# Optimization experiments

Hardware: AMD Instinct MI355X
Metric: run time of the kernel (lower is better)

The kernel has to match this reference:

```python
import jax, jax.numpy as jnp
import numpy as np

NUM_BLOCKS = 4
BLOCK_SIZE = 2048
BATCH = 512
NUM_ITERATIONS = 2
# static tridiagonal block sparsity pattern: (out_block_i, in_block_j)
BLOCK_PAIRS = [(0, 0), (0, 1), (1, 0), (1, 1), (1, 2), (2, 1), (2, 2), (2, 3), (3, 2), (3, 3)]


def setup_inputs() -> dict:
    key = jax.random.key(0)
    kx, kw, kb = jax.random.split(key, 3)
    X = jax.random.normal(kx, (NUM_BLOCKS, BATCH, BLOCK_SIZE), dtype=jnp.float32)
    # torch nn.Linear default init: U(-1/sqrt(fan_in), 1/sqrt(fan_in))
    bound = 1.0 / np.sqrt(BLOCK_SIZE)
    W = jax.random.uniform(kw, (len(BLOCK_PAIRS), BLOCK_SIZE, BLOCK_SIZE),
                           minval=-bound, maxval=bound, dtype=jnp.float32)
    b = jax.random.uniform(kb, (len(BLOCK_PAIRS), BLOCK_SIZE),
                           minval=-bound, maxval=bound, dtype=jnp.float32)
    return {"X": X, "W": W, "b": b}


def reference(X, W, b):
    # X: [num_blocks, batch, block_size]
    # W: [n_present_blocks, out_feat, in_feat], b: [n_present_blocks, out_feat]
    # Each iteration: y_i = relu( sum_{j : (i,j) present} x_j @ W_ij^T + b_ij )
    for _ in range(NUM_ITERATIONS):
        Y = jnp.zeros_like(X)
        for k, (i, j) in enumerate(BLOCK_PAIRS):  # small static set of block GEMMs
            Y = Y.at[i].add(jnp.einsum('be,oe->bo', X[j], W[k]) + b[k])
        X = jax.nn.relu(Y)
    return X
```

## Files before the change

kernel.cpp:

```cpp
#include <hip/hip_runtime.h>
#include <cstdint>
#include <cstddef>

typedef __bf16 bf16;
typedef bf16 bf16x4 __attribute__((ext_vector_type(4)));
typedef bf16 bf16x8 __attribute__((ext_vector_type(8)));
typedef float f32x4 __attribute__((ext_vector_type(4)));

#define NB 4
#define BATCH 512
#define BS 2048
#define NPAIRS 10

__constant__ int c_npairs[NB]   = {2, 3, 3, 2};
__constant__ int c_pj[NB][3]    = {{0, 1, 0}, {0, 1, 2}, {1, 2, 3}, {2, 3, 0}};
__constant__ int c_pk[NB][3]    = {{0, 1, 0}, {2, 3, 4}, {5, 6, 7}, {8, 9, 0}};

__global__ __launch_bounds__(256) void convert_kernel(
    const float* __restrict__ X, const float* __restrict__ W,
    const float* __restrict__ b,
    bf16* __restrict__ Xbf, bf16* __restrict__ Wbf, float* __restrict__ bias4)
{
    const int nW4 = NPAIRS * BS * BS / 4;
    const int nX4 = NB * BATCH * BS / 4;
    int idx    = blockIdx.x * blockDim.x + threadIdx.x;
    int stride = gridDim.x * blockDim.x;
    const float4* W4 = (const float4*)W;
    const float4* X4 = (const float4*)X;
    for (int i = idx; i < nW4; i += stride) {
        float4 v = W4[i];
        bf16x4 o = { (bf16)v.x, (bf16)v.y, (bf16)v.z, (bf16)v.w };
        *(bf16x4*)(Wbf + 4 * (size_t)i) = o;
    }
    for (int i = idx; i < nX4; i += stride) {
        float4 v = X4[i];
        bf16x4 o = { (bf16)v.x, (bf16)v.y, (bf16)v.z, (bf16)v.w };
        *(bf16x4*)(Xbf + 4 * (size_t)i) = o;
    }
    if (idx < NB * BS) {
        int i = idx >> 11;
        int o = idx & (BS - 1);
        float s = 0.f;
        int np = c_npairs[i];
        for (int p = 0; p < np; ++p) s += b[c_pk[i][p] * BS + o];
        bias4[idx] = s;
    }
}

typedef __attribute__((address_space(1))) void void_g;
typedef __attribute__((address_space(3))) void void_l;

__device__ __forceinline__ void gload16(const bf16* g, bf16* l)
{
    __builtin_amdgcn_global_load_lds((void_g*)g, (void_l*)l, 16, 0, 0);
}

__global__ __launch_bounds__(256, 2) void block_gemm(
    const bf16* __restrict__ Xbf,
    const bf16* __restrict__ Wbf,
    const float* __restrict__ bias4,
    bf16* __restrict__ Xnext,
    float* __restrict__ Yout,
    int write_f32)
{
    __shared__ bf16 sA[128 * 32];
    __shared__ bf16 sB[128 * 32];

    const int tid  = threadIdx.x;
    const int lane = tid & 63;
    const int wid  = tid >> 6;
    const int wm   = (wid & 1) * 64;
    const int wn   = (wid >> 1) * 64;
    const int ib   = blockIdx.z;
    const int bm0  = blockIdx.y * 128;
    const int bn0  = blockIdx.x * 128;

    f32x4 acc[4][4];
    const f32x4 zero = {0.f, 0.f, 0.f, 0.f};
#pragma unroll
    for (int i = 0; i < 4; ++i)
#pragma unroll
        for (int j = 0; j < 4; ++j) acc[i][j] = zero;

    const int srow = tid >> 2;
    const int skp  = (tid & 3) * 8;
    bf16* ldsA0 = sA + (size_t)tid * 8;
    bf16* ldsA1 = sA + 2048 + (size_t)tid * 8;
    bf16* ldsB0 = sB + (size_t)tid * 8;
    bf16* ldsB1 = sB + 2048 + (size_t)tid * 8;

    const int lm = lane & 15;
    const int lk = (lane >> 4) * 8;

    const int np = c_npairs[ib];
    for (int p = 0; p < np; ++p) {
        const bf16* Ab = Xbf + ((size_t)c_pj[ib][p] * BATCH + bm0 + srow) * BS + skp;
        const bf16* Bb = Wbf + ((size_t)c_pk[ib][p] * BS    + bn0 + srow) * BS + skp;
        for (int k0 = 0; k0 < BS; k0 += 32) {
            __syncthreads();
            gload16(Ab + k0,            ldsA0);
            gload16(Ab + 64 * BS + k0,  ldsA1);
            gload16(Bb + k0,            ldsB0);
            gload16(Bb + 64 * BS + k0,  ldsB1);
            __syncthreads();

            bf16x8 af[4], bfr[4];
#pragma unroll
            for (int mi = 0; mi < 4; ++mi)
                af[mi] = *(const bf16x8*)(sA + (wm + mi * 16 + lm) * 32 + lk);
#pragma unroll
            for (int ni = 0; ni < 4; ++ni)
                bfr[ni] = *(const bf16x8*)(sB + (wn + ni * 16 + lm) * 32 + lk);
#pragma unroll
            for (int mi = 0; mi < 4; ++mi)
#pragma unroll
                for (int ni = 0; ni < 4; ++ni)
                    acc[mi][ni] = __builtin_amdgcn_mfma_f32_16x16x32_bf16(
                        af[mi], bfr[ni], acc[mi][ni], 0, 0, 0);
        }
    }

    const float* bias = bias4 + ib * BS;
#pragma unroll
    for (int mi = 0; mi < 4; ++mi) {
#pragma unroll
        for (int ni = 0; ni < 4; ++ni) {
            const int m = bm0 + wm + mi * 16 + (lane >> 4) * 4;
            const int n = bn0 + wn + ni * 16 + lm;
            const float bv = bias[n];
            const size_t base = ((size_t)ib * BATCH + m) * BS + n;
            if (write_f32) {
#pragma unroll
                for (int r = 0; r < 4; ++r) {
                    float v = acc[mi][ni][r] + bv;
                    Yout[base + (size_t)r * BS] = v > 0.f ? v : 0.f;
                }
            } else {
#pragma unroll
                for (int r = 0; r < 4; ++r) {
                    float v = acc[mi][ni][r] + bv;
                    v = v > 0.f ? v : 0.f;
                    Xnext[base + (size_t)r * BS] = (bf16)v;
                }
            }
        }
    }
}

extern "C" void kernel_launch(void* const* d_in, const int* in_sizes, int n_in,
                              void* d_out, int out_size, void* d_ws, size_t ws_size,
                              hipStream_t stream)
{
    const float* X = (const float*)d_in[0];
    const float* W = (const float*)d_in[1];
    const float* b = (const float*)d_in[2];
    float* out = (float*)d_out;
    char* ws = (char*)d_ws;

    const size_t W_BYTES = (size_t)NPAIRS * BS * BS * 2;
    const size_t X_BYTES = (size_t)NB * BATCH * BS * 2;

    bf16*  Wbf   = (bf16*)ws;
    bf16*  Xbf0  = (bf16*)(ws + W_BYTES);
    bf16*  Xbf1  = (bf16*)(ws + W_BYTES + X_BYTES);
    float* bias4 = (float*)(ws + W_BYTES + 2 * X_BYTES);

    hipLaunchKernelGGL(convert_kernel, dim3(4096), dim3(256), 0, stream,
                       X, W, b, Xbf0, Wbf, bias4);

    dim3 grid(BS / 128, BATCH / 128, NB);
    hipLaunchKernelGGL(block_gemm, grid, dim3(256), 0, stream,
                       Xbf0, Wbf, bias4, Xbf1, (float*)nullptr, 0);
    hipLaunchKernelGGL(block_gemm, grid, dim3(256), 0, stream,
                       Xbf1, Wbf, bias4, (bf16*)nullptr, out, 1);
}
```

Baseline: 470.5 us.

## Split-K GEMM with in-kernel fp32 W conversion and double-buffered LDS

Drops the separate fp32-to-bf16 conversion pass over W. The GEMM now reads fp32 W directly and converts it in registers before storing to LDS. The K dimension is split four ways, giving four times as many workgroups to fill the device, and the LDS staging is double-buffered so the next tile's loads overlap the current MFMAs. A new combine kernel sums the partials and applies bias and ReLU. The cost is a large fp32 partial buffer written and re-read every iteration, and W is read twice in fp32 instead of once in fp32 plus twice in bf16.

```diff
diff --git a/kernel.cpp b/kernel.cpp
--- a/kernel.cpp
+++ b/kernel.cpp
@@ -10,39 +10,27 @@
 #define NB 4
 #define BATCH 512
 #define BS 2048
-#define NPAIRS 10
-
-__constant__ int c_npairs[NB]   = {2, 3, 3, 2};
-__constant__ int c_pj[NB][3]    = {{0, 1, 0}, {0, 1, 2}, {1, 2, 3}, {2, 3, 0}};
-__constant__ int c_pk[NB][3]    = {{0, 1, 0}, {2, 3, 4}, {5, 6, 7}, {8, 9, 0}};
-
-__global__ __launch_bounds__(256) void convert_kernel(
-    const float* __restrict__ X, const float* __restrict__ W,
-    const float* __restrict__ b,
-    bf16* __restrict__ Xbf, bf16* __restrict__ Wbf, float* __restrict__ bias4)
-{
-    const int nW4 = NPAIRS * BS * BS / 4;
-    const int nX4 = NB * BATCH * BS / 4;
-    int idx    = blockIdx.x * blockDim.x + threadIdx.x;
-    int stride = gridDim.x * blockDim.x;
-    const float4* W4 = (const float4*)W;
-    const float4* X4 = (const float4*)X;
-    for (int i = idx; i < nW4; i += stride) {
-        float4 v = W4[i];
-        bf16x4 o = { (bf16)v.x, (bf16)v.y, (bf16)v.z, (bf16)v.w };
-        *(bf16x4*)(Wbf + 4 * (size_t)i) = o;
-    }
-    for (int i = idx; i < nX4; i += stride) {
-        float4 v = X4[i];
-        bf16x4 o = { (bf16)v.x, (bf16)v.y, (bf16)v.z, (bf16)v.w };
-        *(bf16x4*)(Xbf + 4 * (size_t)i) = o;
-    }
+#define KQ 4
+#define KSPAN (BS / KQ)
+
+__constant__ int c_npairs[NB] = {2, 3, 3, 2};
+__constant__ int c_pj[NB][3]  = {{0, 1, 0}, {0, 1, 2}, {1, 2, 3}, {2, 3, 0}};
+__constant__ int c_pk[NB][3]  = {{0, 1, 0}, {2, 3, 4}, {5, 6, 7}, {8, 9, 0}};
+
+__global__ __launch_bounds__(256) void xcvt_kernel(
+    const float* __restrict__ X, const float* __restrict__ b,
+    bf16* __restrict__ Xbf, float* __restrict__ bias4)
+{
+    const int idx = blockIdx.x * 256 + threadIdx.x;
+    float4 v = ((const float4*)X)[idx];
+    bf16x4 o = { (bf16)v.x, (bf16)v.y, (bf16)v.z, (bf16)v.w };
+    *(bf16x4*)(Xbf + 4 * (size_t)idx) = o;
     if (idx < NB * BS) {
         int i = idx >> 11;
-        int o = idx & (BS - 1);
+        int o2 = idx & (BS - 1);
         float s = 0.f;
         int np = c_npairs[i];
-        for (int p = 0; p < np; ++p) s += b[c_pk[i][p] * BS + o];
+        for (int p = 0; p < np; ++p) s += b[c_pk[i][p] * BS + o2];
         bias4[idx] = s;
     }
 }
@@ -50,30 +38,41 @@
 typedef __attribute__((address_space(1))) void void_g;
 typedef __attribute__((address_space(3))) void void_l;
 
-__device__ __forceinline__ void gload16(const bf16* g, bf16* l)
-{
-    __builtin_amdgcn_global_load_lds((void_g*)g, (void_l*)l, 16, 0, 0);
-}
-
-__global__ __launch_bounds__(256, 2) void block_gemm(
+__global__ __launch_bounds__(256, 4) void gemm_ksplit(
     const bf16* __restrict__ Xbf,
-    const bf16* __restrict__ Wbf,
-    const float* __restrict__ bias4,
-    bf16* __restrict__ Xnext,
-    float* __restrict__ Yout,
-    int write_f32)
-{
-    __shared__ bf16 sA[128 * 32];
-    __shared__ bf16 sB[128 * 32];
+    const float* __restrict__ W,
+    float* __restrict__ P)
+{
+    __shared__ bf16 sA[2][128 * 32];
+    __shared__ bf16 sB[2][128 * 32];
 
     const int tid  = threadIdx.x;
     const int lane = tid & 63;
     const int wid  = tid >> 6;
     const int wm   = (wid & 1) * 64;
     const int wn   = (wid >> 1) * 64;
-    const int ib   = blockIdx.z;
+    const int z    = blockIdx.z;
+    const int ib   = z >> 2;
+    const int kq   = z & 3;
     const int bm0  = blockIdx.y * 128;
     const int bn0  = blockIdx.x * 128;
+    const int np     = c_npairs[ib];
+    const int nsteps = np * (KSPAN / 32);
+
+    const int a_row = tid >> 2;
+    const int a_kp  = (tid & 3) * 8;
+    const int b_row = tid >> 1;
+    const int b_kp  = (tid & 1) * 16;
+
+    const bf16* A_0 = Xbf + ((size_t)c_pj[ib][0] * BATCH + bm0 + a_row) * BS + kq * KSPAN + a_kp;
+    const bf16* A_1 = Xbf + ((size_t)c_pj[ib][1] * BATCH + bm0 + a_row) * BS + kq * KSPAN + a_kp;
+    const bf16* A_2 = Xbf + ((size_t)c_pj[ib][2] * BATCH + bm0 + a_row) * BS + kq * KSPAN + a_kp;
+    const float* B_0 = W + ((size_t)c_pk[ib][0] * BS + bn0 + b_row) * BS + kq * KSPAN + b_kp;
+    const float* B_1 = W + ((size_t)c_pk[ib][1] * BS + bn0 + b_row) * BS + kq * KSPAN + b_kp;
+    const float* B_2 = W + ((size_t)c_pk[ib][2] * BS + bn0 + b_row) * BS + kq * KSPAN + b_kp;
+
+    const int lm = lane & 15;
+    const int lk = (lane >> 4) * 8;
 
     f32x4 acc[4][4];
     const f32x4 zero = {0.f, 0.f, 0.f, 0.f};
@@ -82,68 +81,104 @@
 #pragma unroll
         for (int j = 0; j < 4; ++j) acc[i][j] = zero;
 
-    const int srow = tid >> 2;
-    const int skp  = (tid & 3) * 8;
-    bf16* ldsA0 = sA + (size_t)tid * 8;
-    bf16* ldsA1 = sA + 2048 + (size_t)tid * 8;
-    bf16* ldsB0 = sB + (size_t)tid * 8;
-    bf16* ldsB1 = sB + 2048 + (size_t)tid * 8;
-
-    const int lm = lane & 15;
-    const int lk = (lane >> 4) * 8;
-
-    const int np = c_npairs[ib];
-    for (int p = 0; p < np; ++p) {
-        const bf16* Ab = Xbf + ((size_t)c_pj[ib][p] * BATCH + bm0 + srow) * BS + skp;
-        const bf16* Bb = Wbf + ((size_t)c_pk[ib][p] * BS    + bn0 + srow) * BS + skp;
-        for (int k0 = 0; k0 < BS; k0 += 32) {
-            __syncthreads();
-            gload16(Ab + k0,            ldsA0);
-            gload16(Ab + 64 * BS + k0,  ldsA1);
-            gload16(Bb + k0,            ldsB0);
-            gload16(Bb + 64 * BS + k0,  ldsB1);
-            __syncthreads();
-
-            bf16x8 af[4], bfr[4];
-#pragma unroll
-            for (int mi = 0; mi < 4; ++mi)
-                af[mi] = *(const bf16x8*)(sA + (wm + mi * 16 + lm) * 32 + lk);
+    float4 br0, br1, br2, br3;
+
+    auto stageA = [&](int s, int buf) {
+        const int p = s >> 4;
+        const bf16* Ab = (p == 0) ? A_0 : ((p == 1) ? A_1 : A_2);
+        Ab += (s & 15) * 32;
+        bf16* l = &sA[buf][tid * 8];
+        __builtin_amdgcn_global_load_lds((void_g*)Ab, (void_l*)l, 16, 0, 0);
+        __builtin_amdgcn_global_load_lds((void_g*)(Ab + 64 * BS), (void_l*)(l + 2048), 16, 0, 0);
+    };
+    auto loadB = [&](int s) {
+        const int p = s >> 4;
+        const float* Bb = (p == 0) ? B_0 : ((p == 1) ? B_1 : B_2);
+        Bb += (s & 15) * 32;
+        br0 = *(const float4*)(Bb);
+        br1 = *(const float4*)(Bb + 4);
+        br2 = *(const float4*)(Bb + 8);
+        br3 = *(const float4*)(Bb + 12);
+    };
+    auto commitB = [&](int buf) {
+        bf16x8 w0 = { (bf16)br0.x, (bf16)br0.y, (bf16)br0.z, (bf16)br0.w,
+                      (bf16)br1.x, (bf16)br1.y, (bf16)br1.z, (bf16)br1.w };
+        bf16x8 w1 = { (bf16)br2.x, (bf16)br2.y, (bf16)br2.z, (bf16)br2.w,
+                      (bf16)br3.x, (bf16)br3.y, (bf16)br3.z, (bf16)br3.w };
+        *(bf16x8*)(&sB[buf][b_row * 32 + b_kp])     = w0;
+        *(bf16x8*)(&sB[buf][b_row * 32 + b_kp + 8]) = w1;
+    };
+
+    stageA(0, 0);
+    loadB(0);
+    commitB(0);
+
+    int cur = 0;
+    for (int s = 0; s < nsteps; ++s) {
+        __syncthreads();
+        if (s + 1 < nsteps) {
+            stageA(s + 1, cur ^ 1);
+            loadB(s + 1);
+        }
+        bf16x8 af[4], bfr[4];
+#pragma unroll
+        for (int mi = 0; mi < 4; ++mi)
+            af[mi] = *(const bf16x8*)(&sA[cur][(wm + mi * 16 + lm) * 32 + lk]);
+#pragma unroll
+        for (int ni = 0; ni < 4; ++ni)
+            bfr[ni] = *(const bf16x8*)(&sB[cur][(wn + ni * 16 + lm) * 32 + lk]);
+#pragma unroll
+        for (int mi = 0; mi < 4; ++mi)
 #pragma unroll
             for (int ni = 0; ni < 4; ++ni)
-                bfr[ni] = *(const bf16x8*)(sB + (wn + ni * 16 + lm) * 32 + lk);
-#pragma unroll
-            for (int mi = 0; mi < 4; ++mi)
-#pragma unroll
-                for (int ni = 0; ni < 4; ++ni)
-                    acc[mi][ni] = __builtin_amdgcn_mfma_f32_16x16x32_bf16(
-                        af[mi], bfr[ni], acc[mi][ni], 0, 0, 0);
+                acc[mi][ni] = __builtin_amdgcn_mfma_f32_16x16x32_bf16(
+                    af[mi], bfr[ni], acc[mi][ni], 0, 0, 0);
+        if (s + 1 < nsteps) commitB(cur ^ 1);
+        cur ^= 1;
+    }
+
+    float* Pt = P + ((size_t)z * BATCH + bm0) * BS + bn0;
+#pragma unroll
+    for (int mi = 0; mi < 4; ++mi) {
+#pragma unroll
+        for (int ni = 0; ni < 4; ++ni) {
+            const int m = wm + mi * 16 + (lane >> 4) * 4;
+            const int n = wn + ni * 16 + lm;
+#pragma unroll
+            for (int r = 0; r < 4; ++r)
+                Pt[(size_t)(m + r) * BS + n] = acc[mi][ni][r];
         }
     }
-
-    const float* bias = bias4 + ib * BS;
-#pragma unroll
-    for (int mi = 0; mi < 4; ++mi) {
-#pragma unroll
-        for (int ni = 0; ni < 4; ++ni) {
-            const int m = bm0 + wm + mi * 16 + (lane >> 4) * 4;
-            const int n = bn0 + wn + ni * 16 + lm;
-            const float bv = bias[n];
-            const size_t base = ((size_t)ib * BATCH + m) * BS + n;
-            if (write_f32) {
-#pragma unroll
-                for (int r = 0; r < 4; ++r) {
-                    float v = acc[mi][ni][r] + bv;
-                    Yout[base + (size_t)r * BS] = v > 0.f ? v : 0.f;
-                }
-            } else {
-#pragma unroll
-                for (int r = 0; r < 4; ++r) {
-                    float v = acc[mi][ni][r] + bv;
-                    v = v > 0.f ? v : 0.f;
-                    Xnext[base + (size_t)r * BS] = (bf16)v;
-                }
-            }
-        }
+}
+
+__global__ __launch_bounds__(256) void combine_kernel(
+    const float* __restrict__ P, const float* __restrict__ bias4,
+    bf16* __restrict__ Xnext, float* __restrict__ Yout, int write_f32)
+{
+    const int e4 = blockIdx.x * 256 + threadIdx.x;
+    const int ib  = e4 >> 18;
+    const int loc = e4 & 262143;
+    const float4* Pb = (const float4*)P + (size_t)(ib * 4) * 262144 + loc;
+    float4 p0 = Pb[0];
+    float4 p1 = Pb[262144];
+    float4 p2 = Pb[2 * 262144];
+    float4 p3 = Pb[3 * 262144];
+    const int n4 = e4 & 511;
+    float4 bv = ((const float4*)bias4)[ib * 512 + n4];
+    float sx = p0.x + p1.x + p2.x + p3.x + bv.x;
+    float sy = p0.y + p1.y + p2.y + p3.y + bv.y;
+    float sz = p0.z + p1.z + p2.z + p3.z + bv.z;
+    float sw = p0.w + p1.w + p2.w + p3.w + bv.w;
+    sx = sx > 0.f ? sx : 0.f;
+    sy = sy > 0.f ? sy : 0.f;
+    sz = sz > 0.f ? sz : 0.f;
+    sw = sw > 0.f ? sw : 0.f;
+    if (write_f32) {
+        float4 o = { sx, sy, sz, sw };
+        ((float4*)Yout)[e4] = o;
+    } else {
+        bf16x4 o = { (bf16)sx, (bf16)sy, (bf16)sz, (bf16)sw };
+        *(bf16x4*)(Xnext + 4 * (size_t)e4) = o;
     }
 }
 
@@ -157,20 +192,22 @@
     float* out = (float*)d_out;
     char* ws = (char*)d_ws;
 
-    const size_t W_BYTES = (size_t)NPAIRS * BS * BS * 2;
-    const size_t X_BYTES = (size_t)NB * BATCH * BS * 2;
-
-    bf16*  Wbf   = (bf16*)ws;
-    bf16*  Xbf0  = (bf16*)(ws + W_BYTES);
-    bf16*  Xbf1  = (bf16*)(ws + W_BYTES + X_BYTES);
-    float* bias4 = (float*)(ws + W_BYTES + 2 * X_BYTES);
-
-    hipLaunchKernelGGL(convert_kernel, dim3(4096), dim3(256), 0, stream,
-                       X, W, b, Xbf0, Wbf, bias4);
-
-    dim3 grid(BS / 128, BATCH / 128, NB);
-    hipLaunchKernelGGL(block_gemm, grid, dim3(256), 0, stream,
-                       Xbf0, Wbf, bias4, Xbf1, (float*)nullptr, 0);
-    hipLaunchKernelGGL(block_gemm, grid, dim3(256), 0, stream,
-                       Xbf1, Wbf, bias4, (bf16*)nullptr, out, 1);
-}
+    const size_t XBF_BYTES = (size_t)NB * BATCH * BS * 2;
+    const size_t P_BYTES   = (size_t)NB * KQ * BATCH * BS * 4;
+
+    bf16*  Xbf0  = (bf16*)ws;
+    bf16*  Xbf1  = (bf16*)(ws + XBF_BYTES);
+    float* P     = (float*)(ws + 2 * XBF_BYTES);
+    float* bias4 = (float*)(ws + 2 * XBF_BYTES + P_BYTES);
+
+    hipLaunchKernelGGL(xcvt_kernel, dim3(4096), dim3(256), 0, stream,
+                       X, b, Xbf0, bias4);
+
+    dim3 grid(BS / 128, BATCH / 128, NB * KQ);
+    hipLaunchKernelGGL(gemm_ksplit, grid, dim3(256), 0, stream, Xbf0, W, P);
+    hipLaunchKernelGGL(combine_kernel, dim3(4096), dim3(256), 0, stream,
+                       P, bias4, Xbf1, (float*)nullptr, 0);
+    hipLaunchKernelGGL(gemm_ksplit, grid, dim3(256), 0, stream, Xbf1, W, P);
+    hipLaunchKernelGGL(combine_kernel, dim3(4096), dim3(256), 0, stream,
+                       P, bias4, (bf16*)nullptr, out, 1);
+}
```

Result: faster. 417.8 us (-11.2%).

## Split-K the block GEMM into four partial sums with a separate combine kernel

Applied to the files above, without the earlier changes.

Each block GEMM's K dimension is split into four quarters, so the grid grows from 256 to 1024 workgroups with launch bounds raised to 4 waves per SIMD. Partial fp32 results go to a workspace buffer, and a new combine kernel sums them, adds bias and applies ReLU. The convert kernel's grid is also widened to 8192 blocks so the X conversion runs in a single pass. The aim is to fill the 256 CUs, which the original 256-tile grid underused, at the cost of writing and reading roughly 64 MB of partials per iteration plus two extra launches.

```diff
diff --git a/kernel.cpp b/kernel.cpp
--- a/kernel.cpp
+++ b/kernel.cpp
@@ -11,20 +11,22 @@
 #define BATCH 512
 #define BS 2048
 #define NPAIRS 10
-
-__constant__ int c_npairs[NB]   = {2, 3, 3, 2};
-__constant__ int c_pj[NB][3]    = {{0, 1, 0}, {0, 1, 2}, {1, 2, 3}, {2, 3, 0}};
-__constant__ int c_pk[NB][3]    = {{0, 1, 0}, {2, 3, 4}, {5, 6, 7}, {8, 9, 0}};
-
-__global__ __launch_bounds__(256) void convert_kernel(
+#define KQ 4
+#define KSPAN (BS / KQ)
+
+__constant__ int c_npairs[NB] = {2, 3, 3, 2};
+__constant__ int c_pj[NB][3]  = {{0, 1, 0}, {0, 1, 2}, {1, 2, 3}, {2, 3, 0}};
+__constant__ int c_pk[NB][3]  = {{0, 1, 0}, {2, 3, 4}, {5, 6, 7}, {8, 9, 0}};
+
+__global__ __launch_bounds__(256) void cvt_kernel(
     const float* __restrict__ X, const float* __restrict__ W,
     const float* __restrict__ b,
     bf16* __restrict__ Xbf, bf16* __restrict__ Wbf, float* __restrict__ bias4)
 {
     const int nW4 = NPAIRS * BS * BS / 4;
     const int nX4 = NB * BATCH * BS / 4;
-    int idx    = blockIdx.x * blockDim.x + threadIdx.x;
-    int stride = gridDim.x * blockDim.x;
+    int idx    = blockIdx.x * 256 + threadIdx.x;
+    int stride = 8192 * 256;
     const float4* W4 = (const float4*)W;
     const float4* X4 = (const float4*)X;
     for (int i = idx; i < nW4; i += stride) {
@@ -32,17 +34,17 @@
         bf16x4 o = { (bf16)v.x, (bf16)v.y, (bf16)v.z, (bf16)v.w };
         *(bf16x4*)(Wbf + 4 * (size_t)i) = o;
     }
-    for (int i = idx; i < nX4; i += stride) {
-        float4 v = X4[i];
+    if (idx < nX4) {
+        float4 v = X4[idx];
         bf16x4 o = { (bf16)v.x, (bf16)v.y, (bf16)v.z, (bf16)v.w };
-        *(bf16x4*)(Xbf + 4 * (size_t)i) = o;
+        *(bf16x4*)(Xbf + 4 * (size_t)idx) = o;
     }
     if (idx < NB * BS) {
         int i = idx >> 11;
-        int o = idx & (BS - 1);
+        int o2 = idx & (BS - 1);
         float s = 0.f;
         int np = c_npairs[i];
-        for (int p = 0; p < np; ++p) s += b[c_pk[i][p] * BS + o];
+        for (int p = 0; p < np; ++p) s += b[c_pk[i][p] * BS + o2];
         bias4[idx] = s;
     }
 }
@@ -55,13 +57,10 @@
     __builtin_amdgcn_global_load_lds((void_g*)g, (void_l*)l, 16, 0, 0);
 }
 
-__global__ __launch_bounds__(256, 2) void block_gemm(
+__global__ __launch_bounds__(256, 4) void gemm_ksplit(
     const bf16* __restrict__ Xbf,
     const bf16* __restrict__ Wbf,
-    const float* __restrict__ bias4,
-    bf16* __restrict__ Xnext,
-    float* __restrict__ Yout,
-    int write_f32)
+    float* __restrict__ P)
 {
     __shared__ bf16 sA[128 * 32];
     __shared__ bf16 sB[128 * 32];
@@ -71,7 +70,9 @@
     const int wid  = tid >> 6;
     const int wm   = (wid & 1) * 64;
     const int wn   = (wid >> 1) * 64;
-    const int ib   = blockIdx.z;
+    const int z    = blockIdx.z;
+    const int ib   = z >> 2;
+    const int kq   = z & 3;
     const int bm0  = blockIdx.y * 128;
     const int bn0  = blockIdx.x * 128;
 
@@ -94,9 +95,11 @@
 
     const int np = c_npairs[ib];
     for (int p = 0; p < np; ++p) {
-        const bf16* Ab = Xbf + ((size_t)c_pj[ib][p] * BATCH + bm0 + srow) * BS + skp;
-        const bf16* Bb = Wbf + ((size_t)c_pk[ib][p] * BS    + bn0 + srow) * BS + skp;
-        for (int k0 = 0; k0 < BS; k0 += 32) {
+        const bf16* Ab = Xbf + ((size_t)c_pj[ib][p] * BATCH + bm0 + srow) * BS
+                             + kq * KSPAN + skp;
+        const bf16* Bb = Wbf + ((size_t)c_pk[ib][p] * BS    + bn0 + srow) * BS
+                             + kq * KSPAN + skp;
+        for (int k0 = 0; k0 < KSPAN; k0 += 32) {
             __syncthreads();
             gload16(Ab + k0,            ldsA0);
             gload16(Ab + 64 * BS + k0,  ldsA1);
@@ -120,30 +123,48 @@
         }
     }
 
-    const float* bias = bias4 + ib * BS;
+    float* Pt = P + ((size_t)z * BATCH + bm0) * BS + bn0;
 #pragma unroll
     for (int mi = 0; mi < 4; ++mi) {
 #pragma unroll
         for (int ni = 0; ni < 4; ++ni) {
-            const int m = bm0 + wm + mi * 16 + (lane >> 4) * 4;
-            const int n = bn0 + wn + ni * 16 + lm;
-            const float bv = bias[n];
-            const size_t base = ((size_t)ib * BATCH + m) * BS + n;
-            if (write_f32) {
-#pragma unroll
-                for (int r = 0; r < 4; ++r) {
-                    float v = acc[mi][ni][r] + bv;
-                    Yout[base + (size_t)r * BS] = v > 0.f ? v : 0.f;
-                }
-            } else {
-#pragma unroll
-                for (int r = 0; r < 4; ++r) {
-                    float v = acc[mi][ni][r] + bv;
-                    v = v > 0.f ? v : 0.f;
-                    Xnext[base + (size_t)r * BS] = (bf16)v;
-                }
-            }
+            const int m = wm + mi * 16 + (lane >> 4) * 4;
+            const int n = wn + ni * 16 + lm;
+#pragma unroll
+            for (int r = 0; r < 4; ++r)
+                Pt[(size_t)(m + r) * BS + n] = acc[mi][ni][r];
         }
+    }
+}
+
+__global__ __launch_bounds__(256) void combine_kernel(
+    const float* __restrict__ P, const float* __restrict__ bias4,
+    bf16* __restrict__ Xnext, float* __restrict__ Yout, int write_f32)
+{
+    const int e4 = blockIdx.x * 256 + threadIdx.x;
+    const int ib  = e4 >> 18;
+    const int loc = e4 & 262143;
+    const float4* Pb = (const float4*)P + (size_t)(ib * KQ) * 262144 + loc;
+    float4 p0 = Pb[0];
+    float4 p1 = Pb[262144];
+    float4 p2 = Pb[2 * 262144];
+    float4 p3 = Pb[3 * 262144];
+    const int n4 = e4 & 511;
+    float4 bv = ((const float4*)bias4)[ib * 512 + n4];
+    float sx = p0.x + p1.x + p2.x + p3.x + bv.x;
+    float sy = p0.y + p1.y + p2.y + p3.y + bv.y;
+    float sz = p0.z + p1.z + p2.z + p3.z + bv.z;
+    float sw = p0.w + p1.w + p2.w + p3.w + bv.w;
+    sx = sx > 0.f ? sx : 0.f;
+    sy = sy > 0.f ? sy : 0.f;
+    sz = sz > 0.f ? sz : 0.f;
+    sw = sw > 0.f ? sw : 0.f;
+    if (write_f32) {
+        float4 o = { sx, sy, sz, sw };
+        ((float4*)Yout)[e4] = o;
+    } else {
+        bf16x4 o = { (bf16)sx, (bf16)sy, (bf16)sz, (bf16)sw };
+        *(bf16x4*)(Xnext + 4 * (size_t)e4) = o;
     }
 }
 
@@ -157,20 +178,24 @@
     float* out = (float*)d_out;
     char* ws = (char*)d_ws;
 
-    const size_t W_BYTES = (size_t)NPAIRS * BS * BS * 2;
-    const size_t X_BYTES = (size_t)NB * BATCH * BS * 2;
+    const size_t W_BYTES   = (size_t)NPAIRS * BS * BS * 2;
+    const size_t XBF_BYTES = (size_t)NB * BATCH * BS * 2;
+    const size_t P_BYTES   = (size_t)NB * KQ * BATCH * BS * 4;
 
     bf16*  Wbf   = (bf16*)ws;
     bf16*  Xbf0  = (bf16*)(ws + W_BYTES);
-    bf16*  Xbf1  = (bf16*)(ws + W_BYTES + X_BYTES);
-    float* bias4 = (float*)(ws + W_BYTES + 2 * X_BYTES);
-
-    hipLaunchKernelGGL(convert_kernel, dim3(4096), dim3(256), 0, stream,
+    bf16*  Xbf1  = (bf16*)(ws + W_BYTES + XBF_BYTES);
+    float* P     = (float*)(ws + W_BYTES + 2 * XBF_BYTES);
+    float* bias4 = (float*)(ws + W_BYTES + 2 * XBF_BYTES + P_BYTES);
+
+    hipLaunchKernelGGL(cvt_kernel, dim3(8192), dim3(256), 0, stream,
                        X, W, b, Xbf0, Wbf, bias4);
 
-    dim3 grid(BS / 128, BATCH / 128, NB);
-    hipLaunchKernelGGL(block_gemm, grid, dim3(256), 0, stream,
-                       Xbf0, Wbf, bias4, Xbf1, (float*)nullptr, 0);
-    hipLaunchKernelGGL(block_gemm, grid, dim3(256), 0, stream,
-                       Xbf1, Wbf, bias4, (bf16*)nullptr, out, 1);
-}
+    dim3 grid(BS / 128, BATCH / 128, NB * KQ);
+    hipLaunchKernelGGL(gemm_ksplit, grid, dim3(256), 0, stream, Xbf0, Wbf, P);
+    hipLaunchKernelGGL(combine_kernel, dim3(4096), dim3(256), 0, stream,
+                       P, bias4, Xbf1, (float*)nullptr, 0);
+    hipLaunchKernelGGL(gemm_ksplit, grid, dim3(256), 0, stream, Xbf1, Wbf, P);
+    hipLaunchKernelGGL(combine_kernel, dim3(4096), dim3(256), 0, stream,
+                       P, bias4, (bf16*)nullptr, out, 1);
+}
```

Result: faster. 386.6 us (-17.8%).
